# Kernel tuning notes

Measured on AMD Instinct MI355X. Metric: run time of the kernel, lower is better.

The kernel has to match this reference:

```python
import jax, jax.numpy as jnp
import numpy as np

H = 768
I = 3072
E = 8
B, S = 2, 512
EPS = 1e-12


def setup_inputs() -> dict:
    key = jax.random.key(0)
    ks = jax.random.split(key, 8)
    hidden_states = jax.random.normal(ks[0], (B, S, H), dtype=jnp.float32)
    expert_idx = jax.random.randint(ks[1], (B * S,), 0, E)
    scale1 = 1.0 / np.sqrt(H)
    scale2 = 1.0 / np.sqrt(I)
    W1 = jax.random.uniform(ks[2], (E, H, I), jnp.float32, -scale1, scale1)
    b1 = jax.random.uniform(ks[3], (E, I), jnp.float32, -scale1, scale1)
    W2 = jax.random.uniform(ks[4], (E, I, H), jnp.float32, -scale2, scale2)
    b2 = jax.random.uniform(ks[5], (E, H), jnp.float32, -scale2, scale2)
    gamma = jnp.ones((H,), jnp.float32)
    beta = jnp.zeros((H,), jnp.float32)
    return {
        "hidden_states": hidden_states,
        "expert_idx": expert_idx,
        "W1": W1, "b1": b1, "W2": W2, "b2": b2,
        "gamma": gamma, "beta": beta,
    }


def _moe_ln(hidden_states, expert_idx, W1, b1, W2, b2, gamma, beta):
    b, s, h = hidden_states.shape
    x = hidden_states.reshape(-1, h)  # [T, H]
    out = jnp.zeros_like(x)
    # loop over the small fixed expert count; select per-token results by mask
    for e in range(E):
        inter = jax.nn.gelu(x @ W1[e] + b1[e], approximate=False)
        y_e = inter @ W2[e] + b2[e]
        out = jnp.where((expert_idx == e)[:, None], y_e, out)
    y = out.reshape(b, s, h) + hidden_states  # residual
    mu = jnp.mean(y, axis=-1, keepdims=True)
    var = jnp.mean(jnp.square(y - mu), axis=-1, keepdims=True)
    return (y - mu) * jax.lax.rsqrt(var + EPS) * gamma + beta


def reference(hidden_states, expert_idx, W1, b1, W2, b2, gamma, beta):
    return _moe_ln(hidden_states, expert_idx, W1, b1, W2, b2, gamma, beta)
```

## Files before the change

kernel.cpp:

```cpp
#include <hip/hip_runtime.h>
#include <math.h>

#define T_TOK 1024
#define H_DIM 768
#define I_DIM 3072
#define E_NUM 8
#define BM    128
#define BN    64
#define BK    64
#define MSLOTS 16
#define KSPLIT2 4
#define CONV_Y 8
#define NCONVB (48 * CONV_Y)
#define CONV_CHUNKS (E_NUM * I_DIM * H_DIM / 8)
#define CONV_PER_T (CONV_CHUNKS / (NCONVB * 512))

typedef __attribute__((ext_vector_type(8))) short  short8;
typedef __attribute__((ext_vector_type(4))) float  f32x4;

__device__ __forceinline__ unsigned short f2bf(float f) {
  union { float f; unsigned u; } a; a.f = f;
  unsigned r = a.u + 0x7FFFu + ((a.u >> 16) & 1u);
  return (unsigned short)(r >> 16);
}
__device__ __forceinline__ float gelu_exact(float x) {
  return 0.5f * x * (1.0f + erff(x * 0.70710678118654752f));
}
__device__ __forceinline__ int swz(int row, int k) {
  return row * BK + (k ^ ((row & 7) << 3));
}
__device__ __forceinline__ void gll16(const void* g, void* l) {
  __builtin_amdgcn_global_load_lds(
      (const __attribute__((address_space(1))) void*)g,
      (__attribute__((address_space(3))) void*)l, 16, 0, 0);
}

__global__ __launch_bounds__(1024) void route_kernel(
    const int* __restrict__ eidx, int* __restrict__ perm,
    int* __restrict__ tile_e, int* __restrict__ tile_row,
    int* __restrict__ tile_len, int* __restrict__ ntiles) {
  __shared__ int wcnt[16][E_NUM];
  __shared__ int wpre[16][E_NUM];
  __shared__ int offsh[E_NUM + 1];
  const int t = threadIdx.x;
  const int lane = t & 63, wave = t >> 6;
  const int e = eidx[t];
  unsigned long long myMask = 0;
#pragma unroll
  for (int ee = 0; ee < E_NUM; ++ee) {
    unsigned long long m = __ballot(e == ee);
    if (ee == e) myMask = m;
    if (lane == 0) wcnt[wave][ee] = __popcll(m);
  }
  const int rank = __popcll(myMask & ((1ull << lane) - 1ull));
  __syncthreads();
  if (t < 16 * E_NUM) {
    const int w = t >> 3, ee = t & 7;
    int p = 0;
    for (int w2 = 0; w2 < w; ++w2) p += wcnt[w2][ee];
    wpre[w][ee] = p;
  }
  __syncthreads();
  if (t <= E_NUM) {
    int off = 0;
    for (int ee = 0; ee < t; ++ee) off += wpre[15][ee] + wcnt[15][ee];
    offsh[t] = off;
  }
  __syncthreads();
  perm[offsh[e] + wpre[wave][e] + rank] = t;
  if (t == 0) {
    int n = 0;
    for (int ee = 0; ee < E_NUM; ++ee)
      for (int r = offsh[ee]; r < offsh[ee + 1]; r += BM) {
        tile_e[n] = ee; tile_row[n] = r;
        tile_len[n] = min(offsh[ee + 1] - r, BM); ++n;
      }
    *ntiles = n;
    for (int i = n; i < MSLOTS; ++i) { tile_e[i] = 0; tile_row[i] = 0; tile_len[i] = 0; }
  }
}

__global__ void gather_kernel(const float* __restrict__ x,
                              const int* __restrict__ perm,
                              unsigned short* __restrict__ xg) {
  const int idx = blockIdx.x * 256 + threadIdx.x;
  if (idx >= T_TOK * (H_DIM / 8)) return;
  const int p = idx / (H_DIM / 8);
  const int c = (idx % (H_DIM / 8)) * 8;
  const int t = perm[p];
  const float* src = x + (size_t)t * H_DIM + c;
  const float4 v0 = *(const float4*)(src);
  const float4 v1 = *(const float4*)(src + 4);
  short8 o;
  o[0] = (short)f2bf(v0.x); o[1] = (short)f2bf(v0.y);
  o[2] = (short)f2bf(v0.z); o[3] = (short)f2bf(v0.w);
  o[4] = (short)f2bf(v1.x); o[5] = (short)f2bf(v1.y);
  o[6] = (short)f2bf(v1.z); o[7] = (short)f2bf(v1.w);
  *(short8*)(xg + (size_t)p * H_DIM + c) = o;
}

template <int N_FULL, int K_FULL, int KLOOP, bool IS_FFN1, bool B_BF16>
__global__ __launch_bounds__(512, 4) void moe_gemm(
    const unsigned short* __restrict__ A,
    const void* __restrict__ Wv,
    const float* __restrict__ bias,
    const int* __restrict__ tile_e, const int* __restrict__ tile_row,
    const int* __restrict__ tile_len, const int* __restrict__ ntiles,
    unsigned short* __restrict__ out_bf,
    float* __restrict__ part,
    const float* __restrict__ convSrc,
    unsigned short* __restrict__ convDst) {
  constexpr int KT = KLOOP / BK;
  const int tid  = threadIdx.x;
  const int slot = blockIdx.y;

  if constexpr (IS_FFN1) {
    if (slot >= MSLOTS) {
      const int cb  = blockIdx.x + 48 * (slot - MSLOTS);
      const int lin = cb * 512 + tid;
      const float4* s4 = (const float4*)convSrc;
      short8* d8 = (short8*)convDst;
#pragma unroll
      for (int j = 0; j < CONV_PER_T; ++j) {
        const int idx = j * (NCONVB * 512) + lin;
        const float4 a = s4[2 * idx], b = s4[2 * idx + 1];
        short8 o;
        o[0] = (short)f2bf(a.x); o[1] = (short)f2bf(a.y);
        o[2] = (short)f2bf(a.z); o[3] = (short)f2bf(a.w);
        o[4] = (short)f2bf(b.x); o[5] = (short)f2bf(b.y);
        o[6] = (short)f2bf(b.z); o[7] = (short)f2bf(b.w);
        d8[idx] = o;
      }
      return;
    }
  }
  if (slot >= *ntiles) return;
  const int e    = tile_e[slot];
  const int row0 = tile_row[slot];
  const int len  = tile_len[slot];
  const int n0   = blockIdx.x * BN;
  const int kbase = blockIdx.z * KLOOP;

  __shared__ unsigned short As[2][BM * BK];
  __shared__ unsigned short Bs[2][BN * BK];

  const int lane = tid & 63;
  const int wave = tid >> 6;
  const int wm = wave >> 1, wn = wave & 1;
  const int lr = lane & 15;
  const int lk = (lane >> 4) * 8;

  const unsigned short* agsrc[2];
  int aoff[2];
#pragma unroll
  for (int i = 0; i < 2; ++i) {
    const int c = tid + i * 512;
    const int r = c >> 3, kc = (c & 7) << 3;
    int grow = row0 + r; grow = grow < T_TOK ? grow : (T_TOK - 1);
    agsrc[i] = A + (size_t)grow * K_FULL + kbase + (kc ^ ((r & 7) << 3));
    aoff[i]  = ((tid & ~63) + i * 512) * 8;
  }
  const int bn_ = tid & 63, kb8 = (tid >> 6) * 8;
  const float* wpf = nullptr; const unsigned short* wph = nullptr;
  if constexpr (B_BF16)
    wph = (const unsigned short*)Wv + (size_t)e * K_FULL * N_FULL +
          (size_t)(kbase + kb8) * N_FULL + n0 + bn_;
  else
    wpf = (const float*)Wv + (size_t)e * K_FULL * N_FULL +
          (size_t)(kbase + kb8) * N_FULL + n0 + bn_;

  f32x4 acc[2][2] = {};
  float bregA[8], bregB[8];
  unsigned short uregA[8], uregB[8];

  auto issueA = [&](int kt, int buf) {
#pragma unroll
    for (int i = 0; i < 2; ++i)
      gll16(agsrc[i] + kt * BK, &As[buf][aoff[i]]);
  };
  auto loadB = [&](int kt, float* bf, unsigned short* bh) {
#pragma unroll
    for (int j = 0; j < 8; ++j) {
      if constexpr (B_BF16) bh[j] = wph[(size_t)(kt * BK + j) * N_FULL];
      else                  bf[j] = wpf[(size_t)(kt * BK + j) * N_FULL];
    }
  };
  auto writeB = [&](int buf, const float* bf, const unsigned short* bh) {
    short8 p;
#pragma unroll
    for (int j = 0; j < 8; ++j)
      p[j] = B_BF16 ? (short)bh[j] : (short)f2bf(bf[j]);
    *(short8*)(&Bs[buf][swz(bn_, kb8)]) = p;
  };
  auto mfma_tile = [&](int buf) {
#pragma unroll
    for (int ks = 0; ks < 2; ++ks) {
      const int kk = ks * 32 + lk;
      short8 af[2], bfr[2];
#pragma unroll
      for (int m = 0; m < 2; ++m)
        af[m] = *(const short8*)(&As[buf][swz(wm * 32 + m * 16 + lr, kk)]);
#pragma unroll
      for (int n = 0; n < 2; ++n)
        bfr[n] = *(const short8*)(&Bs[buf][swz(wn * 32 + n * 16 + lr, kk)]);
#pragma unroll
      for (int m = 0; m < 2; ++m)
#pragma unroll
        for (int n = 0; n < 2; ++n)
          acc[m][n] = __builtin_amdgcn_mfma_f32_16x16x32_bf16(af[m], bfr[n], acc[m][n], 0, 0, 0);
    }
  };

  issueA(0, 0); loadB(0, bregA, uregA);
#pragma unroll 1
  for (int kt = 0; kt < KT; kt += 2) {
    asm volatile("s_waitcnt vmcnt(0)" ::: "memory");
    writeB(0, bregA, uregA);
    asm volatile("s_waitcnt lgkmcnt(0)" ::: "memory");
    __builtin_amdgcn_s_barrier();
    __builtin_amdgcn_sched_barrier(0);
    issueA(kt + 1, 1); loadB(kt + 1, bregB, uregB);
    mfma_tile(0);
    asm volatile("s_waitcnt vmcnt(0)" ::: "memory");
    writeB(1, bregB, uregB);
    asm volatile("s_waitcnt lgkmcnt(0)" ::: "memory");
    __builtin_amdgcn_s_barrier();
    __builtin_amdgcn_sched_barrier(0);
    if (kt + 2 < KT) { issueA(kt + 2, 0); loadB(kt + 2, bregA, uregA); }
    mfma_tile(1);
  }

#pragma unroll
  for (int n = 0; n < 2; ++n) {
    const int gc = n0 + wn * 32 + n * 16 + lr;
    float bv = 0.f;
    if constexpr (IS_FFN1) bv = bias[(size_t)e * N_FULL + gc];
#pragma unroll
    for (int m = 0; m < 2; ++m) {
      const int rbase = wm * 32 + m * 16 + (lane >> 4) * 4;
#pragma unroll
      for (int j = 0; j < 4; ++j) {
        const int rl = rbase + j;
        if (rl < len) {
          if constexpr (IS_FFN1) {
            out_bf[(size_t)(row0 + rl) * N_FULL + gc] = f2bf(gelu_exact(acc[m][n][j] + bv));
          } else {
            part[((size_t)blockIdx.z * T_TOK + row0 + rl) * N_FULL + gc] = acc[m][n][j];
          }
        }
      }
    }
  }
}

__global__ void ln_kernel(const float* __restrict__ part,
                          const float* __restrict__ x,
                          const int* __restrict__ perm,
                          const int* __restrict__ eidx,
                          const float* __restrict__ b2,
                          const float* __restrict__ gamma,
                          const float* __restrict__ beta,
                          float* __restrict__ out) {
  const int p = blockIdx.x;
  const int tid = threadIdx.x;
  const int t = perm[p];
  const int e = eidx[t];
  float v[3], s = 0.f, ss = 0.f;
#pragma unroll
  for (int i = 0; i < 3; ++i) {
    const int c = tid + i * 256;
    float a = x[(size_t)t * H_DIM + c] + b2[(size_t)e * H_DIM + c];
#pragma unroll
    for (int s4 = 0; s4 < KSPLIT2; ++s4)
      a += part[((size_t)s4 * T_TOK + p) * H_DIM + c];
    v[i] = a; s += a; ss += a * a;
  }
#pragma unroll
  for (int o = 32; o; o >>= 1) { s += __shfl_down(s, o); ss += __shfl_down(ss, o); }
  __shared__ float ps[4], pss[4];
  __shared__ float mu_s, ir_s;
  const int w = tid >> 6;
  if ((tid & 63) == 0) { ps[w] = s; pss[w] = ss; }
  __syncthreads();
  if (tid == 0) {
    const float S = ps[0] + ps[1] + ps[2] + ps[3];
    const float SS = pss[0] + pss[1] + pss[2] + pss[3];
    const float mu = S * (1.0f / H_DIM);
    const float var = SS * (1.0f / H_DIM) - mu * mu;
    mu_s = mu; ir_s = rsqrtf(var + 1e-12f);
  }
  __syncthreads();
  const float mu = mu_s, ir = ir_s;
#pragma unroll
  for (int i = 0; i < 3; ++i) {
    const int c = tid + i * 256;
    out[(size_t)t * H_DIM + c] = (v[i] - mu) * ir * gamma[c] + beta[c];
  }
}

extern "C" void kernel_launch(void* const* d_in, const int* in_sizes, int n_in,
                              void* d_out, int out_size, void* d_ws, size_t ws_size,
                              hipStream_t stream) {
  const float* x     = (const float*)d_in[0];
  const int*   eidx  = (const int*)d_in[1];
  const float* W1    = (const float*)d_in[2];
  const float* b1    = (const float*)d_in[3];
  const float* W2    = (const float*)d_in[4];
  const float* b2    = (const float*)d_in[5];
  const float* gamma = (const float*)d_in[6];
  const float* beta  = (const float*)d_in[7];
  float* out = (float*)d_out;

  char* ws = (char*)d_ws;
  int* perm     = (int*)(ws);
  int* tile_e   = (int*)(ws + 4096);
  int* tile_row = (int*)(ws + 4352);
  int* tile_len = (int*)(ws + 4608);
  int* ntiles   = (int*)(ws + 4864);
  size_t off = 8192;
  unsigned short* xg = (unsigned short*)(ws + off);  off += (size_t)2 * T_TOK * H_DIM;
  unsigned short* inter = (unsigned short*)(ws + off); off += (size_t)2 * T_TOK * I_DIM;
  float* part = (float*)(ws + off); off += (size_t)4 * KSPLIT2 * T_TOK * H_DIM;
  unsigned short* w2bf = (unsigned short*)(ws + off);
  const size_t need = off + (size_t)2 * E_NUM * I_DIM * H_DIM;
  const bool useBF = ws_size >= need;

  route_kernel<<<1, T_TOK, 0, stream>>>(eidx, perm, tile_e, tile_row, tile_len, ntiles);
  gather_kernel<<<(T_TOK * (H_DIM / 8) + 255) / 256, 256, 0, stream>>>(x, perm, xg);
  if (useBF) {
    moe_gemm<I_DIM, H_DIM, H_DIM, true, false>
        <<<dim3(I_DIM / BN, MSLOTS + CONV_Y, 1), 512, 0, stream>>>(
        xg, W1, b1, tile_e, tile_row, tile_len, ntiles, inter, nullptr, W2, w2bf);
    moe_gemm<H_DIM, I_DIM, I_DIM / KSPLIT2, false, true>
        <<<dim3(H_DIM / BN, MSLOTS, KSPLIT2), 512, 0, stream>>>(
        inter, w2bf, nullptr, tile_e, tile_row, tile_len, ntiles, nullptr, part,
        nullptr, nullptr);
  } else {
    moe_gemm<I_DIM, H_DIM, H_DIM, true, false>
        <<<dim3(I_DIM / BN, MSLOTS, 1), 512, 0, stream>>>(
        xg, W1, b1, tile_e, tile_row, tile_len, ntiles, inter, nullptr, nullptr, nullptr);
    moe_gemm<H_DIM, I_DIM, I_DIM / KSPLIT2, false, false>
        <<<dim3(H_DIM / BN, MSLOTS, KSPLIT2), 512, 0, stream>>>(
        inter, W2, nullptr, tile_e, tile_row, tile_len, ntiles, nullptr, part,
        nullptr, nullptr);
  }
  ln_kernel<<<T_TOK, 256, 0, stream>>>(part, x, perm, eidx, b2, gamma, beta, out);
  (void)in_sizes; (void)n_in; (void)out_size;
}
```

Baseline: 73.65 us.

## Pre-convert W1 to bf16 and deepen B-load prefetch pipeline

Adds a separate kernel that converts all of W1 to bf16 before FFN1, so FFN1 reads bf16 weights while W2 is still converted by the extra blocks in the FFN1 grid. The GEMM main loop is restructured so each phase waits with vmcnt(8) instead of a full drain, and B loads are issued two k-tiles ahead. The aim is to halve FFN1 weight traffic and keep global loads in flight across barriers. The cost is an extra full fp32 read and bf16 write of W1 on every call, plus more registers held for in-flight loads.

New measurement: 88.37 us. 1.2x slower.

```diff
diff --git a/kernel.cpp b/kernel.cpp
--- a/kernel.cpp
+++ b/kernel.cpp
@@ -99,6 +99,20 @@
   *(short8*)(xg + (size_t)p * H_DIM + c) = o;
 }
 
+__global__ __launch_bounds__(512) void cvt_kernel(
+    const float* __restrict__ src, unsigned short* __restrict__ dst) {
+  const int idx = blockIdx.x * 512 + threadIdx.x;
+  if (idx >= CONV_CHUNKS) return;
+  const float4 a = ((const float4*)src)[2 * idx];
+  const float4 b = ((const float4*)src)[2 * idx + 1];
+  short8 o;
+  o[0] = (short)f2bf(a.x); o[1] = (short)f2bf(a.y);
+  o[2] = (short)f2bf(a.z); o[3] = (short)f2bf(a.w);
+  o[4] = (short)f2bf(b.x); o[5] = (short)f2bf(b.y);
+  o[6] = (short)f2bf(b.z); o[7] = (short)f2bf(b.w);
+  ((short8*)dst)[idx] = o;
+}
+
 template <int N_FULL, int K_FULL, int KLOOP, bool IS_FFN1, bool B_BF16>
 __global__ __launch_bounds__(512, 4) void moe_gemm(
     const unsigned short* __restrict__ A,
@@ -114,7 +128,7 @@
   const int tid  = threadIdx.x;
   const int slot = blockIdx.y;
 
-  if constexpr (IS_FFN1) {
+  if constexpr (IS_FFN1 && B_BF16) {
     if (slot >= MSLOTS) {
       const int cb  = blockIdx.x + 48 * (slot - MSLOTS);
       const int lin = cb * 512 + tid;
@@ -160,49 +174,50 @@
     agsrc[i] = A + (size_t)grow * K_FULL + kbase + (kc ^ ((r & 7) << 3));
     aoff[i]  = ((tid & ~63) + i * 512) * 8;
   }
-  const int bn_ = tid & 63, kb8 = (tid >> 6) * 8;
-  const float* wpf = nullptr; const unsigned short* wph = nullptr;
+  const int bn_ = tid & 63;
+  const int kb8 = (tid >> 6) * 8;
+  const float* wpF = nullptr; const unsigned short* wpH = nullptr;
   if constexpr (B_BF16)
-    wph = (const unsigned short*)Wv + (size_t)e * K_FULL * N_FULL +
+    wpH = (const unsigned short*)Wv + (size_t)e * K_FULL * N_FULL +
           (size_t)(kbase + kb8) * N_FULL + n0 + bn_;
   else
-    wpf = (const float*)Wv + (size_t)e * K_FULL * N_FULL +
+    wpF = (const float*)Wv + (size_t)e * K_FULL * N_FULL +
           (size_t)(kbase + kb8) * N_FULL + n0 + bn_;
 
   f32x4 acc[2][2] = {};
-  float bregA[8], bregB[8];
-  unsigned short uregA[8], uregB[8];
+  float Xf[8], Yf[8];
+  unsigned short Xh[8], Yh[8];
 
   auto issueA = [&](int kt, int buf) {
 #pragma unroll
     for (int i = 0; i < 2; ++i)
       gll16(agsrc[i] + kt * BK, &As[buf][aoff[i]]);
   };
-  auto loadB = [&](int kt, float* bf, unsigned short* bh) {
+  auto loadB = [&](int kt, float* df, unsigned short* dh) {
 #pragma unroll
     for (int j = 0; j < 8; ++j) {
-      if constexpr (B_BF16) bh[j] = wph[(size_t)(kt * BK + j) * N_FULL];
-      else                  bf[j] = wpf[(size_t)(kt * BK + j) * N_FULL];
+      if constexpr (B_BF16) dh[j] = wpH[(size_t)(kt * BK + j) * N_FULL];
+      else                  df[j] = wpF[(size_t)(kt * BK + j) * N_FULL];
     }
   };
-  auto writeB = [&](int buf, const float* bf, const unsigned short* bh) {
+  auto writeB = [&](int buf, const float* df, const unsigned short* dh) {
     short8 p;
 #pragma unroll
     for (int j = 0; j < 8; ++j)
-      p[j] = B_BF16 ? (short)bh[j] : (short)f2bf(bf[j]);
+      p[j] = B_BF16 ? (short)dh[j] : (short)f2bf(df[j]);
     *(short8*)(&Bs[buf][swz(bn_, kb8)]) = p;
   };
   auto mfma_tile = [&](int buf) {
 #pragma unroll
     for (int ks = 0; ks < 2; ++ks) {
-      const int kk = ks * 32 + lk;
+      const int kp = ks * 32 + lk;
       short8 af[2], bfr[2];
 #pragma unroll
       for (int m = 0; m < 2; ++m)
-        af[m] = *(const short8*)(&As[buf][swz(wm * 32 + m * 16 + lr, kk)]);
+        af[m] = *(const short8*)(&As[buf][swz(wm * 32 + m * 16 + lr, kp)]);
 #pragma unroll
       for (int n = 0; n < 2; ++n)
-        bfr[n] = *(const short8*)(&Bs[buf][swz(wn * 32 + n * 16 + lr, kk)]);
+        bfr[n] = *(const short8*)(&Bs[buf][swz(wn * 32 + n * 16 + lr, kp)]);
 #pragma unroll
       for (int m = 0; m < 2; ++m)
 #pragma unroll
@@ -210,25 +225,33 @@
           acc[m][n] = __builtin_amdgcn_mfma_f32_16x16x32_bf16(af[m], bfr[n], acc[m][n], 0, 0, 0);
     }
   };
-
-  issueA(0, 0); loadB(0, bregA, uregA);
-#pragma unroll 1
-  for (int kt = 0; kt < KT; kt += 2) {
-    asm volatile("s_waitcnt vmcnt(0)" ::: "memory");
-    writeB(0, bregA, uregA);
+  auto phase = [&](int t, int buf, float* cf, unsigned short* ch,
+                   bool nextA, bool nextB, bool drain) {
+    if (drain) asm volatile("s_waitcnt vmcnt(0)" ::: "memory");
+    else       asm volatile("s_waitcnt vmcnt(8)" ::: "memory");
+    writeB(buf, cf, ch);
     asm volatile("s_waitcnt lgkmcnt(0)" ::: "memory");
     __builtin_amdgcn_s_barrier();
     __builtin_amdgcn_sched_barrier(0);
-    issueA(kt + 1, 1); loadB(kt + 1, bregB, uregB);
-    mfma_tile(0);
-    asm volatile("s_waitcnt vmcnt(0)" ::: "memory");
-    writeB(1, bregB, uregB);
-    asm volatile("s_waitcnt lgkmcnt(0)" ::: "memory");
-    __builtin_amdgcn_s_barrier();
+    if (nextA) issueA(t + 1, buf ^ 1);
     __builtin_amdgcn_sched_barrier(0);
-    if (kt + 2 < KT) { issueA(kt + 2, 0); loadB(kt + 2, bregA, uregA); }
-    mfma_tile(1);
-  }
+    if (nextB) loadB(t + 2, cf, ch);
+    __builtin_amdgcn_sched_barrier(0);
+    mfma_tile(buf);
+  };
+
+  loadB(0, Xf, Xh);
+  __builtin_amdgcn_sched_barrier(0);
+  issueA(0, 0);
+  __builtin_amdgcn_sched_barrier(0);
+  loadB(1, Yf, Yh);
+#pragma unroll 1
+  for (int t = 0; t < KT - 2; t += 2) {
+    phase(t,     0, Xf, Xh, true, true, false);
+    phase(t + 1, 1, Yf, Yh, true, true, false);
+  }
+  phase(KT - 2, 0, Xf, Xh, true,  false, false);
+  phase(KT - 1, 1, Yf, Yh, false, false, true);
 
 #pragma unroll
   for (int n = 0; n < 2; ++n) {
@@ -318,27 +341,30 @@
   int* tile_len = (int*)(ws + 4608);
   int* ntiles   = (int*)(ws + 4864);
   size_t off = 8192;
-  unsigned short* xg = (unsigned short*)(ws + off);  off += (size_t)2 * T_TOK * H_DIM;
+  unsigned short* xg = (unsigned short*)(ws + off);    off += (size_t)2 * T_TOK * H_DIM;
   unsigned short* inter = (unsigned short*)(ws + off); off += (size_t)2 * T_TOK * I_DIM;
-  float* part = (float*)(ws + off); off += (size_t)4 * KSPLIT2 * T_TOK * H_DIM;
-  unsigned short* w2bf = (unsigned short*)(ws + off);
-  const size_t need = off + (size_t)2 * E_NUM * I_DIM * H_DIM;
-  const bool useBF = ws_size >= need;
+  float* part = (float*)(ws + off);                    off += (size_t)4 * KSPLIT2 * T_TOK * H_DIM;
+  unsigned short* w1b = (unsigned short*)(ws + off);   off += (size_t)2 * E_NUM * H_DIM * I_DIM;
+  unsigned short* w2b = (unsigned short*)(ws + off);
+  const size_t need = off + (size_t)2 * E_NUM * H_DIM * I_DIM;
+  const bool bf = ws_size >= need;
 
   route_kernel<<<1, T_TOK, 0, stream>>>(eidx, perm, tile_e, tile_row, tile_len, ntiles);
   gather_kernel<<<(T_TOK * (H_DIM / 8) + 255) / 256, 256, 0, stream>>>(x, perm, xg);
-  if (useBF) {
-    moe_gemm<I_DIM, H_DIM, H_DIM, true, false>
+  if (bf) {
+    cvt_kernel<<<(CONV_CHUNKS + 511) / 512, 512, 0, stream>>>(W1, w1b);
+    moe_gemm<I_DIM, H_DIM, H_DIM, true, true>
         <<<dim3(I_DIM / BN, MSLOTS + CONV_Y, 1), 512, 0, stream>>>(
-        xg, W1, b1, tile_e, tile_row, tile_len, ntiles, inter, nullptr, W2, w2bf);
+        xg, w1b, b1, tile_e, tile_row, tile_len, ntiles, inter, nullptr, W2, w2b);
     moe_gemm<H_DIM, I_DIM, I_DIM / KSPLIT2, false, true>
         <<<dim3(H_DIM / BN, MSLOTS, KSPLIT2), 512, 0, stream>>>(
-        inter, w2bf, nullptr, tile_e, tile_row, tile_len, ntiles, nullptr, part,
+        inter, w2b, nullptr, tile_e, tile_row, tile_len, ntiles, nullptr, part,
         nullptr, nullptr);
   } else {
     moe_gemm<I_DIM, H_DIM, H_DIM, true, false>
         <<<dim3(I_DIM / BN, MSLOTS, 1), 512, 0, stream>>>(
-        xg, W1, b1, tile_e, tile_row, tile_len, ntiles, inter, nullptr, nullptr, nullptr);
+        xg, W1, b1, tile_e, tile_row, tile_len, ntiles, inter, nullptr,
+        nullptr, nullptr);
     moe_gemm<H_DIM, I_DIM, I_DIM / KSPLIT2, false, false>
         <<<dim3(H_DIM / BN, MSLOTS, KSPLIT2), 512, 0, stream>>>(
         inter, W2, nullptr, tile_e, tile_row, tile_len, ntiles, nullptr, part,
```
